# Performance work log

Measured on AMD Instinct MI355X. Metric: run time of the kernel, lower is better.

Reference implementation:

```python
import jax, jax.numpy as jnp
import numpy as np

DATA_DIM = 128
UNITS = 512
LAYERS = 3
BATCH = 32
IN_STEPS = 1000   # int((T_input + 0.5*dt)//dt)
OUT_STEPS = 100   # int((T_output + 0.5*dt)//dt)


def setup_inputs() -> dict:
    key = jax.random.key(0)
    ks = jax.random.split(key, 16)
    d = {}
    d["x"] = jax.random.normal(ks[0], (BATCH, IN_STEPS, DATA_DIM), jnp.float32)
    in_dims = [DATA_DIM, UNITS, UNITS]
    i = 1
    for j in range(LAYERS):
        d[f"W{j}"] = jax.random.normal(ks[i], (in_dims[j], 3 * UNITS), jnp.float32) * 0.05; i += 1
        d[f"U{j}"] = jax.random.normal(ks[i], (UNITS, 3 * UNITS), jnp.float32) * 0.05; i += 1
        d[f"b{j}"] = jnp.zeros((2, 3 * UNITS), jnp.float32)
        d[f"s{j}"] = jax.random.normal(ks[i], (1, UNITS), jnp.float32); i += 1
    d["Wd"] = jax.random.normal(ks[i], (UNITS, DATA_DIM), jnp.float32) * 0.05
    d["bd"] = jnp.zeros((DATA_DIM,), jnp.float32)
    return d


def _gru_cell(x, h, W, U, b):
    # Keras GRUCell, reset_after=True (TF2 default)
    mx = x @ W + b[0]           # [B, 3U]
    mh = h @ U + b[1]           # [B, 3U]
    xz, xr, xh = jnp.split(mx, 3, axis=-1)
    hz, hr, hh = jnp.split(mh, 3, axis=-1)
    z = jax.nn.sigmoid(xz + hz)
    r = jax.nn.sigmoid(xr + hr)
    cand = jnp.tanh(xh + r * hh)
    return z * h + (1.0 - z) * cand


def reference(x, W0, U0, b0, s0, W1, U1, b1, s1, W2, U2, b2, s2, Wd, bd):
    params = [(W0, U0, b0), (W1, U1, b1), (W2, U2, b2)]
    B = x.shape[0]
    # learnable initial states, tiled over batch -> [L, B, U]
    h0 = jnp.stack([jnp.tile(s, (B, 1)) for s in (s0, s1, s2)])
    # model processes timesteps 0 .. in_steps-2 (last input step unused)
    xs = jnp.swapaxes(x[:, : IN_STEPS - 1, :], 0, 1)  # [T-1, B, D]

    def step(h, xt):
        hs = []
        inp = xt
        for j, (W, U, b) in enumerate(params):
            hj = _gru_cell(inp, h[j], W, U, b)
            hs.append(hj)
            inp = hj
        hn = jnp.stack(hs)  # [L, B, U]
        return hn, (inp, hn)

    _, (ys, hs) = jax.lax.scan(step, h0, xs)
    # outputs correspond to steps in_steps-out_steps-1 .. in_steps-2
    ys = ys[-OUT_STEPS:]   # [out_steps, B, U]
    hs = hs[-OUT_STEPS:]   # [out_steps, L, B, U]
    preds = ys @ Wd + bd   # [out_steps, B, D]
    predictions = jnp.swapaxes(preds, 0, 1)        # [B, out_steps, D]
    hidden = jnp.transpose(hs, (2, 0, 1, 3))       # [B, out_steps, L, U]
    return predictions, hidden
```

## Files before the change

### kernel.cpp

```cpp
#include <hip/hip_runtime.h>
#include <math.h>

#define B_   32
#define INS  1000
#define TS   999
#define D_   128
#define U_   512
#define G3   1536
#define OUTS 100
#define NB   208
#define NTHR 512

#define HBUF_OFF 0
#define HBUF_SZ  (4*3*512*32)
#define RING_OFF HBUF_SZ
#define RING_SZ  (4*1536*32)
#define BAR_OFF  (RING_OFF + RING_SZ)

#define W_CHK1  3080
#define W_CHK0  1544
#define XBUF_OFF 12288
#define PART_OFF 24640
#define SMEM_FLOATS 32384
#define PIDX3(q,g,c,e) ((q)*968 + ((g)*8+(c))*40 + (e))

#define WT_STORE(p, v) __hip_atomic_store((p), (v), __ATOMIC_RELAXED, __HIP_MEMORY_SCOPE_AGENT)
#define CG_LOAD(p)     __hip_atomic_load((p), __ATOMIC_RELAXED, __HIP_MEMORY_SCOPE_AGENT)

#define FMA12() \
  acc[0][0]=fmaf(av.x,w0,acc[0][0]); acc[0][1]=fmaf(av.y,w0,acc[0][1]); \
  acc[0][2]=fmaf(av.z,w0,acc[0][2]); acc[0][3]=fmaf(av.w,w0,acc[0][3]); \
  acc[1][0]=fmaf(av.x,w1,acc[1][0]); acc[1][1]=fmaf(av.y,w1,acc[1][1]); \
  acc[1][2]=fmaf(av.z,w1,acc[1][2]); acc[1][3]=fmaf(av.w,w1,acc[1][3]); \
  acc[2][0]=fmaf(av.x,w2,acc[2][0]); acc[2][1]=fmaf(av.y,w2,acc[2][1]); \
  acc[2][2]=fmaf(av.z,w2,acc[2][2]); acc[2][3]=fmaf(av.w,w2,acc[2][3]);

#define LD16(DST, PTR) { _Pragma("unroll") \
  for (int t_ = 0; t_ < 16; ++t_) DST[t_] = *(const float4*)((PTR) + t_*32); }

#define FMA16(BUF) { _Pragma("unroll") \
  for (int t_ = 0; t_ < 16; ++t_) { \
    const float w0 = wp[0], w1 = wp[1], w2 = wp[2]; \
    const float4 av = BUF[t_]; \
    FMA12(); \
    wp += 24; } }

__global__ void gru_init_kernel(const float* __restrict__ s0,
                                const float* __restrict__ s1,
                                const float* __restrict__ s2,
                                float* __restrict__ ws) {
  int g = blockIdx.x * 256 + threadIdx.x;
  if (g < 4096) { unsigned* bar = (unsigned*)(ws + BAR_OFF); bar[g] = 0u; }
  for (int i = g; i < 3 * 512 * 32; i += gridDim.x * 256) {
    int which = i / (512 * 32);
    int r = i - which * (512 * 32);
    int k = r >> 5, e = r & 31;
    const float* s = (which == 0) ? s0 : ((which == 1) ? s1 : s2);
    ws[HBUF_OFF + 3 * 49152 + which * 16384 + k * 32 + e] = s[k];
  }
}

__device__ __forceinline__ void wait_deps(unsigned* slots, int role, int t) {
  const int tid = threadIdx.x;
  const unsigned* p = nullptr; int tgt = 0;
  if (role < 0) {
    if (tid < 64)       { p = &slots[(0   + tid)       * 16]; tgt = t - 3; }
  } else if (role == 0) {
    if (tid < 64)       { p = &slots[(0   + tid)       * 16]; tgt = t;     }
    else if (tid < 80)  { p = &slots[(192 + tid - 64)  * 16]; tgt = t + 1; }
    else if (tid < 144) { p = &slots[(64  + tid - 80)  * 16]; tgt = t - 3; }
  } else if (role == 1) {
    if (tid < 64)       { p = &slots[(64  + tid)       * 16]; tgt = t;     }
    else if (tid < 128) { p = &slots[(0   + tid - 64)  * 16]; tgt = t + 1; }
    else if (tid < 192) { p = &slots[(128 + tid - 128) * 16]; tgt = t - 3; }
  } else {
    if (tid < 64)       { p = &slots[(128 + tid)       * 16]; tgt = t;     }
    else if (tid < 128) { p = &slots[(64  + tid - 64)  * 16]; tgt = t + 1; }
  }
  if (p && tgt > 0) {
    while ((int)CG_LOAD(p) < tgt) __builtin_amdgcn_s_sleep(1);
  }
  __syncthreads();
  if (role >= 0) {
    if (tid == 0) __builtin_amdgcn_fence(__ATOMIC_ACQUIRE, "agent");
    __syncthreads();
  }
}

__device__ __forceinline__ void publish(unsigned* slots, int sidx, int t) {
  __syncthreads();
  if (threadIdx.x == 0) WT_STORE(&slots[sidx * 16], (unsigned)(t + 1));
}

__global__ __launch_bounds__(NTHR, 1) void gru_persist(
    const float* __restrict__ x,
    const float* __restrict__ W0c, const float* __restrict__ U0c, const float* __restrict__ b0c,
    const float* __restrict__ W1c, const float* __restrict__ U1c, const float* __restrict__ b1c,
    const float* __restrict__ W2c, const float* __restrict__ U2c, const float* __restrict__ b2c,
    const float* __restrict__ Wd, const float* __restrict__ bd,
    float* __restrict__ out, float* __restrict__ ws)
{
  float* hbuf = ws + HBUF_OFF;
  float* ring = ws + RING_OFF;
  unsigned* slots = (unsigned*)(ws + BAR_OFF);
  float* pred_out = out;
  float* hid_out  = out + B_ * OUTS * D_;

  const int bid = blockIdx.x;
  const int tid = threadIdx.x;

  int role, rb;
  if      (bid < 16)  { role = -1; rb = bid; }
  else if (bid < 80)  { role = 0;  rb = bid - 16; }
  else if (bid < 144) { role = 1;  rb = bid - 80; }
  else                { role = 2;  rb = bid - 144; }
  const int sidx = (role < 0) ? (192 + rb) : (role * 64 + rb);

  __shared__ float smem[SMEM_FLOATS];
  float* part = smem + PART_OFF;

  const int eg  = tid & 7;
  const int c_l = (tid >> 3) & 7;
  const int q   = tid >> 6;
  const int cb  = (rb & 7) * 8 + (rb >> 3);
  const int c0  = cb * 8;
  const int rc = tid >> 5;
  const int re = tid & 31;
  const int xb0 = ((rb & 7) * 2 + (rb >> 3)) * 96;
  const int cg3 = (tid & 31) * 3;
  const int e0  = (tid >> 5) * 2;

  const float *Wj = nullptr, *Ujp = nullptr, *bj = nullptr;
  if      (role == 0) { Ujp = U0c; bj = b0c; }
  else if (role == 1) { Wj = W1c; Ujp = U1c; bj = b1c; }
  else if (role == 2) { Wj = W2c; Ujp = U2c; bj = b2c; }

  if (role < 0) {
    for (int idx = tid; idx < 128 * 96; idx += NTHR)
      smem[idx] = W0c[(idx / 96) * G3 + xb0 + (idx % 96)];
    for (int f = tid; f < 1024; f += NTHR) {
      int e = f >> 5, d4 = (f & 31) * 4;
      *(float4*)(smem + XBUF_OFF + e * 128 + d4) =
          *(const float4*)(x + e * (INS * D_) + d4);
    }
  } else {
    const int chunk = (role == 0) ? 64 : 128;
    const int chks  = (role == 0) ? W_CHK0 : W_CHK1;
    const int total = 8 * chunk * 24;
    for (int idx = tid; idx < total; idx += NTHR) {
      int qq = idx / (chunk * 24);
      int r  = idx - qq * (chunk * 24);
      int i  = r / 24;
      int cg = r - i * 24;
      int c  = cg / 3, g = cg - c * 3;
      const float* mat; int row;
      if (role == 0)      { mat = Ujp; row = qq * 64 + i; }
      else if (qq < 4)    { mat = Wj;  row = qq * 128 + i; }
      else                { mat = Ujp; row = (qq - 4) * 128 + i; }
      smem[qq * chks + (i * 8 + c) * 3 + g] = mat[row * G3 + g * 512 + c0 + c];
    }
  }
  float bz = 0.f, br = 0.f, b0h = 0.f, b1h = 0.f;
  if (role >= 0 && tid < 256) {
    const int cg2 = c0 + rc;
    bz  = bj[cg2] + bj[G3 + cg2];
    br  = bj[512 + cg2] + bj[G3 + 512 + cg2];
    b0h = bj[1024 + cg2];
    b1h = bj[G3 + 1024 + cg2];
  }
  __syncthreads();

  for (int t = 0; t < TS; ++t) {
    wait_deps(slots, role, t);

    if (role < 0) {
      float4 xp0, xp1;
      const bool pf = (t + 1) < TS;
      if (pf) {
        int f0 = tid, f1 = tid + 512;
        xp0 = *(const float4*)(x + (f0 >> 5) * (INS * D_) + (t + 1) * D_ + (f0 & 31) * 4);
        xp1 = *(const float4*)(x + (f1 >> 5) * (INS * D_) + (t + 1) * D_ + (f1 & 31) * 4);
      }
      const float* xb = smem + XBUF_OFF + (t & 1) * 4096;
      float acc[3][2];
      #pragma unroll
      for (int c = 0; c < 3; ++c) { acc[c][0] = 0.f; acc[c][1] = 0.f; }
      #pragma unroll 4
      for (int k4 = 0; k4 < D_; k4 += 4) {
        float4 v0 = *(const float4*)(xb + e0 * 128 + k4);
        float4 v1 = *(const float4*)(xb + (e0 + 1) * 128 + k4);
        float xs0[4] = {v0.x, v0.y, v0.z, v0.w};
        float xs1[4] = {v1.x, v1.y, v1.z, v1.w};
        #pragma unroll
        for (int kk = 0; kk < 4; ++kk) {
          const float* wpx = smem + (k4 + kk) * 96 + cg3;
          float w0 = wpx[0], w1 = wpx[1], w2 = wpx[2];
          acc[0][0] = fmaf(xs0[kk], w0, acc[0][0]);
          acc[0][1] = fmaf(xs1[kk], w0, acc[0][1]);
          acc[1][0] = fmaf(xs0[kk], w1, acc[1][0]);
          acc[1][1] = fmaf(xs1[kk], w1, acc[1][1]);
          acc[2][0] = fmaf(xs0[kk], w2, acc[2][0]);
          acc[2][1] = fmaf(xs1[kk], w2, acc[2][1]);
        }
      }
      float* dst = ring + (t & 3) * (G3 * 32);
      #pragma unroll
      for (int c = 0; c < 3; ++c) {
        WT_STORE(dst + (xb0 + cg3 + c) * 32 + e0,     acc[c][0]);
        WT_STORE(dst + (xb0 + cg3 + c) * 32 + e0 + 1, acc[c][1]);
      }
      if (pf) {
        float* xw = smem + XBUF_OFF + ((t + 1) & 1) * 4096;
        int f0 = tid, f1 = tid + 512;
        *(float4*)(xw + (f0 >> 5) * 128 + (f0 & 31) * 4) = xp0;
        *(float4*)(xw + (f1 >> 5) * 128 + (f1 & 31) * 4) = xp1;
      }
    } else {
      const int j = role;
      const float* hown = hbuf + ((t + 3) & 3) * 49152;
      const float* hup  = hbuf + (t & 3) * 49152;
      float xz = 0.f, xr2 = 0.f, xhv0 = 0.f, hp = 0.f;
      if (tid < 256) {
        const int cg2 = c0 + rc;
        hp = hown[j * 16384 + cg2 * 32 + re];
        if (j == 0) {
          const float* r3 = ring + (t & 3) * (G3 * 32);
          xz   = r3[cg2 * 32 + re];
          xr2  = r3[(512 + cg2) * 32 + re];
          xhv0 = r3[(1024 + cg2) * 32 + re];
        }
      }

      float acc[3][4];
      #pragma unroll
      for (int g2 = 0; g2 < 3; ++g2)
        #pragma unroll
        for (int i2 = 0; i2 < 4; ++i2) acc[g2][i2] = 0.f;

      float4 bufA[16], bufB[16], bufC[16];
      if (j == 0) {
        const float* Ab = hown + (q * 64) * 32 + eg * 4;
        const float* wp = smem + q * W_CHK0 + c_l * 3;
        LD16(bufA, Ab);        LD16(bufB, Ab + 512);
        LD16(bufC, Ab + 1024); FMA16(bufA);
        LD16(bufA, Ab + 1536); FMA16(bufB);
        FMA16(bufC);
        FMA16(bufA);
      } else {
        const int kb = (q & 3) * 128;
        const float* Ab = ((q < 4) ? (hup + (j - 1) * 16384) : (hown + j * 16384))
                          + kb * 32 + eg * 4;
        const float* wp = smem + q * W_CHK1 + c_l * 3;
        LD16(bufA, Ab);        LD16(bufB, Ab + 512);
        LD16(bufC, Ab + 1024); FMA16(bufA);
        LD16(bufA, Ab + 1536); FMA16(bufB);
        LD16(bufB, Ab + 2048); FMA16(bufC);
        LD16(bufC, Ab + 2560); FMA16(bufA);
        LD16(bufA, Ab + 3072); FMA16(bufB);
        LD16(bufB, Ab + 3584); FMA16(bufC);
        FMA16(bufA);
        FMA16(bufB);
      }
      #pragma unroll
      for (int g2 = 0; g2 < 3; ++g2) {
        *(float4*)&part[PIDX3(q, g2, c_l, eg * 4)] =
            make_float4(acc[g2][0], acc[g2][1], acc[g2][2], acc[g2][3]);
      }
      __syncthreads();

      if (tid < 256) {
        float gz = 0.f, gr = 0.f, xh = 0.f, hh = 0.f;
        #pragma unroll
        for (int q2 = 0; q2 < 8; ++q2) {
          gz += part[PIDX3(q2, 0, rc, re)];
          gr += part[PIDX3(q2, 1, rc, re)];
          float v = part[PIDX3(q2, 2, rc, re)];
          if (j == 0)       hh += v;
          else if (q2 < 4)  xh += v;
          else              hh += v;
        }
        const int cg2 = c0 + rc;
        const float xhv = (j == 0) ? xhv0 : xh;
        const float zi = gz + xz + bz;
        const float ri = gr + xr2 + br;
        const float z = 1.f / (1.f + expf(-zi));
        const float r = 1.f / (1.f + expf(-ri));
        const float cand = tanhf((xhv + b0h) + r * (hh + b1h));
        const float hn = z * hp + (1.f - z) * cand;
        WT_STORE(&hbuf[(t & 3) * 49152 + j * 16384 + cg2 * 32 + re], hn);
        if (t >= TS - OUTS) {
          WT_STORE(&hid_out[((re * OUTS + (t - (TS - OUTS))) * 3 + j) * U_ + cg2], hn);
        }
      }
    }
    publish(slots, sidx, t);
  }

  if (tid < 64) {
    while ((int)CG_LOAD(&slots[(128 + tid) * 16]) < TS) __builtin_amdgcn_s_sleep(1);
  }
  __syncthreads();
  if (tid == 0) __builtin_amdgcn_fence(__ATOMIC_ACQUIRE, "agent");
  __syncthreads();

  const int gt = bid * NTHR + tid;
  for (int o = gt; o < B_ * OUTS * D_; o += NB * NTHR) {
    int b  = o / (OUTS * D_);
    int r2 = o - b * (OUTS * D_);
    int s  = r2 >> 7;
    int dd = r2 & 127;
    const float* ys = hid_out + ((b * OUTS + s) * 3 + 2) * U_;
    float acc = bd[dd];
    #pragma unroll 4
    for (int k = 0; k < U_; k += 4) {
      float4 yv = *(const float4*)(ys + k);
      acc = fmaf(yv.x, Wd[(k    ) * D_ + dd], acc);
      acc = fmaf(yv.y, Wd[(k + 1) * D_ + dd], acc);
      acc = fmaf(yv.z, Wd[(k + 2) * D_ + dd], acc);
      acc = fmaf(yv.w, Wd[(k + 3) * D_ + dd], acc);
    }
    pred_out[o] = acc;
  }
}

extern "C" void kernel_launch(void* const* d_in, const int* in_sizes, int n_in,
                              void* d_out, int out_size, void* d_ws, size_t ws_size,
                              hipStream_t stream) {
  const float* x  = (const float*)d_in[0];
  const float* W0 = (const float*)d_in[1];
  const float* U0 = (const float*)d_in[2];
  const float* b0 = (const float*)d_in[3];
  const float* s0 = (const float*)d_in[4];
  const float* W1 = (const float*)d_in[5];
  const float* U1 = (const float*)d_in[6];
  const float* b1 = (const float*)d_in[7];
  const float* s1 = (const float*)d_in[8];
  const float* W2 = (const float*)d_in[9];
  const float* U2 = (const float*)d_in[10];
  const float* b2 = (const float*)d_in[11];
  const float* s2 = (const float*)d_in[12];
  const float* Wd = (const float*)d_in[13];
  const float* bd = (const float*)d_in[14];
  float* ws = (float*)d_ws;

  gru_init_kernel<<<192, 256, 0, stream>>>(s0, s1, s2, ws);
  gru_persist<<<NB, NTHR, 0, stream>>>(x, W0, U0, b0, W1, U1, b1,
                                       W2, U2, b2, Wd, bd, (float*)d_out, ws);
}
```

Before: 10.52 ms.

## Add aggregator blocks that fold per-block progress slots into per-layer flags

Four extra blocks are launched. Each one polls the per-block progress slots of one role (the three layers plus the input projection) and publishes a single aggregated per-layer flag. Worker blocks now spin on one or two flag words each instead of having up to 144 threads poll individual slots, and the sleep interval is lengthened. This cuts polling traffic on the shared slots but adds an extra hop of latency on every step's dependency chain. It also needs all 212 blocks to be co-resident, or the aggregators could deadlock.

```diff
diff --git a/kernel.cpp b/kernel.cpp
--- a/kernel.cpp
+++ b/kernel.cpp
@@ -8,7 +8,7 @@
 #define U_   512
 #define G3   1536
 #define OUTS 100
-#define NB   208
+#define NB   212
 #define NTHR 512
 
 #define HBUF_OFF 0
@@ -26,6 +26,7 @@
 
 #define WT_STORE(p, v) __hip_atomic_store((p), (v), __ATOMIC_RELAXED, __HIP_MEMORY_SCOPE_AGENT)
 #define CG_LOAD(p)     __hip_atomic_load((p), __ATOMIC_RELAXED, __HIP_MEMORY_SCOPE_AGENT)
+#define FLAGP(bar, j)  (&(bar)[(216 + (j)) * 16])
 
 #define FMA12() \
   acc[0][0]=fmaf(av.x,w0,acc[0][0]); acc[0][1]=fmaf(av.y,w0,acc[0][1]); \
@@ -60,25 +61,25 @@
   }
 }
 
-__device__ __forceinline__ void wait_deps(unsigned* slots, int role, int t) {
+__device__ __forceinline__ void wait_flags(unsigned* bar, int role, int t) {
   const int tid = threadIdx.x;
   const unsigned* p = nullptr; int tgt = 0;
   if (role < 0) {
-    if (tid < 64)       { p = &slots[(0   + tid)       * 16]; tgt = t - 3; }
+    if (tid == 0)      { p = FLAGP(bar, 0); tgt = t - 3; }
   } else if (role == 0) {
-    if (tid < 64)       { p = &slots[(0   + tid)       * 16]; tgt = t;     }
-    else if (tid < 80)  { p = &slots[(192 + tid - 64)  * 16]; tgt = t + 1; }
-    else if (tid < 144) { p = &slots[(64  + tid - 80)  * 16]; tgt = t - 3; }
+    if (tid == 0)      { p = FLAGP(bar, 0); tgt = t;     }
+    else if (tid == 1) { p = FLAGP(bar, 3); tgt = t + 1; }
+    else if (tid == 2) { p = FLAGP(bar, 1); tgt = t - 3; }
   } else if (role == 1) {
-    if (tid < 64)       { p = &slots[(64  + tid)       * 16]; tgt = t;     }
-    else if (tid < 128) { p = &slots[(0   + tid - 64)  * 16]; tgt = t + 1; }
-    else if (tid < 192) { p = &slots[(128 + tid - 128) * 16]; tgt = t - 3; }
+    if (tid == 0)      { p = FLAGP(bar, 1); tgt = t;     }
+    else if (tid == 1) { p = FLAGP(bar, 0); tgt = t + 1; }
+    else if (tid == 2) { p = FLAGP(bar, 2); tgt = t - 3; }
   } else {
-    if (tid < 64)       { p = &slots[(128 + tid)       * 16]; tgt = t;     }
-    else if (tid < 128) { p = &slots[(64  + tid - 64)  * 16]; tgt = t + 1; }
+    if (tid == 0)      { p = FLAGP(bar, 2); tgt = t;     }
+    else if (tid == 1) { p = FLAGP(bar, 1); tgt = t + 1; }
   }
   if (p && tgt > 0) {
-    while ((int)CG_LOAD(p) < tgt) __builtin_amdgcn_s_sleep(1);
+    while ((int)CG_LOAD(p) < tgt) __builtin_amdgcn_s_sleep(2);
   }
   __syncthreads();
   if (role >= 0) {
@@ -108,6 +109,19 @@
 
   const int bid = blockIdx.x;
   const int tid = threadIdx.x;
+
+  if (bid >= 208) {
+    const int aj   = bid - 208;
+    const int base = (aj < 3) ? aj * 64 : 192;
+    const int n    = (aj < 3) ? 64 : 16;
+    for (int T = 1; T <= TS; ++T) {
+      if (tid < n) {
+        while ((int)CG_LOAD(&slots[(base + tid) * 16]) < T) __builtin_amdgcn_s_sleep(2);
+      }
+      __syncthreads();
+      if (tid == 0) WT_STORE(FLAGP(slots, aj), (unsigned)T);
+    }
+  } else {
 
   int role, rb;
   if      (bid < 16)  { role = -1; rb = bid; }
@@ -171,7 +185,7 @@
   __syncthreads();
 
   for (int t = 0; t < TS; ++t) {
-    wait_deps(slots, role, t);
+    wait_flags(slots, role, t);
 
     if (role < 0) {
       float4 xp0, xp1;
@@ -295,13 +309,17 @@
     }
     publish(slots, sidx, t);
   }
-
-  if (tid < 64) {
-    while ((int)CG_LOAD(&slots[(128 + tid) * 16]) < TS) __builtin_amdgcn_s_sleep(1);
-  }
-  __syncthreads();
-  if (tid == 0) __builtin_amdgcn_fence(__ATOMIC_ACQUIRE, "agent");
-  __syncthreads();
+  }
+
+  {
+    unsigned* slots2 = (unsigned*)(ws + BAR_OFF);
+    if (tid == 0) {
+      while ((int)CG_LOAD(FLAGP(slots2, 2)) < TS) __builtin_amdgcn_s_sleep(2);
+    }
+    __syncthreads();
+    if (tid == 0) __builtin_amdgcn_fence(__ATOMIC_ACQUIRE, "agent");
+    __syncthreads();
+  }
 
   const int gt = bid * NTHR + tid;
   for (int o = gt; o < B_ * OUTS * D_; o += NB * NTHR) {
```

New measurement: 10.87 ms. 3.4% more time.

## Stage hidden-state chunks into LDS via async global_load_lds triple-buffer pipeline

Applied to the files above, without the earlier changes.

The GRU layer blocks no longer load hidden-state operands straight into registers (large float4 register buffers). Each step is split into 2048-float chunks that are copied asynchronously into a three-slot LDS staging ring with global_load_lds, two chunks in flight, and each wave then does the FMAs from LDS. The weight layout is reordered to match the new chunk-by-subgroup reduction, and the partial-sum buffer now carries a separate slot for the input-path and hidden-path candidate sums. This cuts register pressure and overlaps global latency with compute, at the cost of a block barrier per chunk and more LDS use.

```diff
diff --git a/kernel.cpp b/kernel.cpp
--- a/kernel.cpp
+++ b/kernel.cpp
@@ -17,33 +17,44 @@
 #define RING_SZ  (4*1536*32)
 #define BAR_OFF  (RING_OFF + RING_SZ)
 
-#define W_CHK1  3080
-#define W_CHK0  1544
+#define PART_OFF  24576
+#define STAGE_OFF 33792
+#define SMEM_FLOATS 39936
+#define PIDX4(s,g,c,e) ((((s)*4+(g))*8+(c))*36 + (e))
 #define XBUF_OFF 12288
-#define PART_OFF 24640
-#define SMEM_FLOATS 32384
-#define PIDX3(q,g,c,e) ((q)*968 + ((g)*8+(c))*40 + (e))
 
 #define WT_STORE(p, v) __hip_atomic_store((p), (v), __ATOMIC_RELAXED, __HIP_MEMORY_SCOPE_AGENT)
 #define CG_LOAD(p)     __hip_atomic_load((p), __ATOMIC_RELAXED, __HIP_MEMORY_SCOPE_AGENT)
 
-#define FMA12() \
-  acc[0][0]=fmaf(av.x,w0,acc[0][0]); acc[0][1]=fmaf(av.y,w0,acc[0][1]); \
-  acc[0][2]=fmaf(av.z,w0,acc[0][2]); acc[0][3]=fmaf(av.w,w0,acc[0][3]); \
-  acc[1][0]=fmaf(av.x,w1,acc[1][0]); acc[1][1]=fmaf(av.y,w1,acc[1][1]); \
-  acc[1][2]=fmaf(av.z,w1,acc[1][2]); acc[1][3]=fmaf(av.w,w1,acc[1][3]); \
-  acc[2][0]=fmaf(av.x,w2,acc[2][0]); acc[2][1]=fmaf(av.y,w2,acc[2][1]); \
-  acc[2][2]=fmaf(av.z,w2,acc[2][2]); acc[2][3]=fmaf(av.w,w2,acc[2][3]);
-
-#define LD16(DST, PTR) { _Pragma("unroll") \
-  for (int t_ = 0; t_ < 16; ++t_) DST[t_] = *(const float4*)((PTR) + t_*32); }
-
-#define FMA16(BUF) { _Pragma("unroll") \
-  for (int t_ = 0; t_ < 16; ++t_) { \
-    const float w0 = wp[0], w1 = wp[1], w2 = wp[2]; \
-    const float4 av = BUF[t_]; \
-    FMA12(); \
-    wp += 24; } }
+#define GLOAD_LDS(G, L) __builtin_amdgcn_global_load_lds( \
+  (const __attribute__((address_space(1))) void*)(G), \
+  (__attribute__((address_space(3))) void*)(L), 16, 0, 0)
+
+#define WAITV1 do { asm volatile("s_waitcnt vmcnt(1)" ::: "memory"); \
+  __builtin_amdgcn_sched_barrier(0); } while (0)
+#define WAITV0 do { asm volatile("s_waitcnt vmcnt(0)" ::: "memory"); \
+  __builtin_amdgcn_sched_barrier(0); } while (0)
+
+#define CHUNK_FMA(GH) { \
+  const float* bp  = smem + STAGE_OFF + (c % 3) * 2048 + sub * 256 + eg * 4; \
+  const float* wp2 = smem + (c * 64 + sub * 8) * 24 + c_l * 3; \
+  _Pragma("unroll") \
+  for (int rr = 0; rr < 8; ++rr) { \
+    float4 av = *(const float4*)(bp + rr * 32); \
+    float w0 = wp2[0], w1 = wp2[1], w2 = wp2[2]; \
+    az[0]=fmaf(av.x,w0,az[0]); az[1]=fmaf(av.y,w0,az[1]); \
+    az[2]=fmaf(av.z,w0,az[2]); az[3]=fmaf(av.w,w0,az[3]); \
+    ar[0]=fmaf(av.x,w1,ar[0]); ar[1]=fmaf(av.y,w1,ar[1]); \
+    ar[2]=fmaf(av.z,w1,ar[2]); ar[3]=fmaf(av.w,w1,ar[3]); \
+    GH[0]=fmaf(av.x,w2,GH[0]); GH[1]=fmaf(av.y,w2,GH[1]); \
+    GH[2]=fmaf(av.z,w2,GH[2]); GH[3]=fmaf(av.w,w2,GH[3]); \
+    wp2 += 24; \
+  } }
+
+#define ISSUE_CHUNK(SRCBASE, CC) do { \
+  const float* gsrc_ = (SRCBASE) + wv * 256 + lane * 4; \
+  GLOAD_LDS(gsrc_, smem + STAGE_OFF + ((CC) % 3) * 2048 + wv * 256); \
+} while (0)
 
 __global__ void gru_init_kernel(const float* __restrict__ s0,
                                 const float* __restrict__ s1,
@@ -82,7 +93,7 @@
   }
   __syncthreads();
   if (role >= 0) {
-    if (tid == 0) __builtin_amdgcn_fence(__ATOMIC_ACQUIRE, "agent");
+    if (threadIdx.x == 0) __builtin_amdgcn_fence(__ATOMIC_ACQUIRE, "agent");
     __syncthreads();
   }
 }
@@ -121,7 +132,9 @@
 
   const int eg  = tid & 7;
   const int c_l = (tid >> 3) & 7;
-  const int q   = tid >> 6;
+  const int sub = tid >> 6;
+  const int wv  = tid >> 6;
+  const int lane = tid & 63;
   const int cb  = (rb & 7) * 8 + (rb >> 3);
   const int c0  = cb * 8;
   const int rc = tid >> 5;
@@ -143,21 +156,17 @@
       *(float4*)(smem + XBUF_OFF + e * 128 + d4) =
           *(const float4*)(x + e * (INS * D_) + d4);
     }
+  } else if (role == 0) {
+    for (int idx = tid; idx < 512 * 24; idx += NTHR) {
+      int row = idx / 24, cg = idx - row * 24, cc = cg / 3, g = cg - cc * 3;
+      smem[idx] = Ujp[row * G3 + g * 512 + c0 + cc];
+    }
   } else {
-    const int chunk = (role == 0) ? 64 : 128;
-    const int chks  = (role == 0) ? W_CHK0 : W_CHK1;
-    const int total = 8 * chunk * 24;
-    for (int idx = tid; idx < total; idx += NTHR) {
-      int qq = idx / (chunk * 24);
-      int r  = idx - qq * (chunk * 24);
-      int i  = r / 24;
-      int cg = r - i * 24;
-      int c  = cg / 3, g = cg - c * 3;
-      const float* mat; int row;
-      if (role == 0)      { mat = Ujp; row = qq * 64 + i; }
-      else if (qq < 4)    { mat = Wj;  row = qq * 128 + i; }
-      else                { mat = Ujp; row = (qq - 4) * 128 + i; }
-      smem[qq * chks + (i * 8 + c) * 3 + g] = mat[row * G3 + g * 512 + c0 + c];
+    for (int idx = tid; idx < 1024 * 24; idx += NTHR) {
+      int row = idx / 24, cg = idx - row * 24, cc = cg / 3, g = cg - cc * 3;
+      const float* mat = (row < 512) ? Wj : Ujp;
+      int mr = (row < 512) ? row : row - 512;
+      smem[idx] = mat[mr * G3 + g * 512 + c0 + cc];
     }
   }
   float bz = 0.f, br = 0.f, b0h = 0.f, b1h = 0.f;
@@ -217,12 +226,45 @@
       }
     } else {
       const int j = role;
-      const float* hown = hbuf + ((t + 3) & 3) * 49152;
-      const float* hup  = hbuf + (t & 3) * 49152;
+      const float* hownb = hbuf + ((t + 3) & 3) * 49152 + j * 16384;
+      const float* hupb  = (j > 0) ? (hbuf + (t & 3) * 49152 + (j - 1) * 16384)
+                                   : nullptr;
+
+      float az[4] = {0,0,0,0}, ar[4] = {0,0,0,0};
+      float axh[4] = {0,0,0,0}, ahh[4] = {0,0,0,0};
+
+      if (j == 0) {
+        ISSUE_CHUNK(hownb + 0 * 2048, 0);
+        ISSUE_CHUNK(hownb + 1 * 2048, 1);
+        #pragma unroll
+        for (int c = 0; c < 8; ++c) {
+          if (c < 7) WAITV1; else WAITV0;
+          __builtin_amdgcn_s_barrier();
+          __builtin_amdgcn_sched_barrier(0);
+          if (c + 2 < 8) ISSUE_CHUNK(hownb + (c + 2) * 2048, c + 2);
+          CHUNK_FMA(ahh);
+        }
+      } else {
+        ISSUE_CHUNK(hupb + 0 * 2048, 0);
+        ISSUE_CHUNK(hupb + 1 * 2048, 1);
+        #pragma unroll
+        for (int c = 0; c < 16; ++c) {
+          if (c < 15) WAITV1; else WAITV0;
+          __builtin_amdgcn_s_barrier();
+          __builtin_amdgcn_sched_barrier(0);
+          if (c + 2 < 16) {
+            const float* nsrc = (c + 2 < 8) ? (hupb + (c + 2) * 2048)
+                                            : (hownb + (c - 6) * 2048);
+            ISSUE_CHUNK(nsrc, c + 2);
+          }
+          if (c < 8) { CHUNK_FMA(axh); } else { CHUNK_FMA(ahh); }
+        }
+      }
+
       float xz = 0.f, xr2 = 0.f, xhv0 = 0.f, hp = 0.f;
       if (tid < 256) {
         const int cg2 = c0 + rc;
-        hp = hown[j * 16384 + cg2 * 32 + re];
+        hp = hownb[cg2 * 32 + re];
         if (j == 0) {
           const float* r3 = ring + (t & 3) * (G3 * 32);
           xz   = r3[cg2 * 32 + re];
@@ -231,53 +273,28 @@
         }
       }
 
-      float acc[3][4];
-      #pragma unroll
-      for (int g2 = 0; g2 < 3; ++g2)
-        #pragma unroll
-        for (int i2 = 0; i2 < 4; ++i2) acc[g2][i2] = 0.f;
-
-      float4 bufA[16], bufB[16], bufC[16];
+      *(float4*)&part[PIDX4(sub, 0, c_l, eg * 4)] = make_float4(az[0], az[1], az[2], az[3]);
+      *(float4*)&part[PIDX4(sub, 1, c_l, eg * 4)] = make_float4(ar[0], ar[1], ar[2], ar[3]);
       if (j == 0) {
-        const float* Ab = hown + (q * 64) * 32 + eg * 4;
-        const float* wp = smem + q * W_CHK0 + c_l * 3;
-        LD16(bufA, Ab);        LD16(bufB, Ab + 512);
-        LD16(bufC, Ab + 1024); FMA16(bufA);
-        LD16(bufA, Ab + 1536); FMA16(bufB);
-        FMA16(bufC);
-        FMA16(bufA);
+        *(float4*)&part[PIDX4(sub, 2, c_l, eg * 4)] = make_float4(ahh[0], ahh[1], ahh[2], ahh[3]);
       } else {
-        const int kb = (q & 3) * 128;
-        const float* Ab = ((q < 4) ? (hup + (j - 1) * 16384) : (hown + j * 16384))
-                          + kb * 32 + eg * 4;
-        const float* wp = smem + q * W_CHK1 + c_l * 3;
-        LD16(bufA, Ab);        LD16(bufB, Ab + 512);
-        LD16(bufC, Ab + 1024); FMA16(bufA);
-        LD16(bufA, Ab + 1536); FMA16(bufB);
-        LD16(bufB, Ab + 2048); FMA16(bufC);
-        LD16(bufC, Ab + 2560); FMA16(bufA);
-        LD16(bufA, Ab + 3072); FMA16(bufB);
-        LD16(bufB, Ab + 3584); FMA16(bufC);
-        FMA16(bufA);
-        FMA16(bufB);
-      }
-      #pragma unroll
-      for (int g2 = 0; g2 < 3; ++g2) {
-        *(float4*)&part[PIDX3(q, g2, c_l, eg * 4)] =
-            make_float4(acc[g2][0], acc[g2][1], acc[g2][2], acc[g2][3]);
+        *(float4*)&part[PIDX4(sub, 2, c_l, eg * 4)] = make_float4(axh[0], axh[1], axh[2], axh[3]);
+        *(float4*)&part[PIDX4(sub, 3, c_l, eg * 4)] = make_float4(ahh[0], ahh[1], ahh[2], ahh[3]);
       }
       __syncthreads();
 
       if (tid < 256) {
         float gz = 0.f, gr = 0.f, xh = 0.f, hh = 0.f;
         #pragma unroll
-        for (int q2 = 0; q2 < 8; ++q2) {
-          gz += part[PIDX3(q2, 0, rc, re)];
-          gr += part[PIDX3(q2, 1, rc, re)];
-          float v = part[PIDX3(q2, 2, rc, re)];
-          if (j == 0)       hh += v;
-          else if (q2 < 4)  xh += v;
-          else              hh += v;
+        for (int s2 = 0; s2 < 8; ++s2) {
+          gz += part[PIDX4(s2, 0, rc, re)];
+          gr += part[PIDX4(s2, 1, rc, re)];
+          if (j == 0) {
+            hh += part[PIDX4(s2, 2, rc, re)];
+          } else {
+            xh += part[PIDX4(s2, 2, rc, re)];
+            hh += part[PIDX4(s2, 3, rc, re)];
+          }
         }
         const int cg2 = c0 + rc;
         const float xhv = (j == 0) ? xhv0 : xh;
```

Result: slower. 11.85 ms (+12.6%).
